# Kernel tuning notes

Measured on AMD Instinct MI355X. Metric: run time of the kernel, lower is better.

The kernel has to match this reference:

```python
import jax, jax.numpy as jnp
import numpy as np

INPUT, LATENT, HIDDEN, LAYERS = 64, 32, 128, 1
N, L = 256, 512


def setup_inputs() -> dict:
    key = jax.random.key(0)
    ks = jax.random.split(key, 12)
    s = 0.02
    inp = {
        "X": jax.random.normal(ks[0], (N, L, INPUT), jnp.float32),
        "eps_z": jax.random.normal(ks[1], (L, LAYERS, N, LATENT), jnp.float32),
        "eps_x": jax.random.normal(ks[2], (L, LAYERS, N, INPUT), jnp.float32),
        # qzcx: NormalModel(input+hidden -> latent): Linear to (mean, raw_std)
        "Wq": s * jax.random.normal(ks[3], (INPUT + HIDDEN, 2 * LATENT), jnp.float32),
        "bq": jnp.zeros((2 * LATENT,), jnp.float32),
        # pxcz: NormalModel(latent+hidden -> input)
        "Wp": s * jax.random.normal(ks[4], (LATENT + HIDDEN, 2 * INPUT), jnp.float32),
        "bp": jnp.zeros((2 * INPUT,), jnp.float32),
        # GRUCell(input+latent -> hidden), gates ordered (r, z, n) as in torch
        "W_ih": s * jax.random.normal(ks[5], (INPUT + LATENT, 3 * HIDDEN), jnp.float32),
        "W_hh": s * jax.random.normal(ks[6], (HIDDEN, 3 * HIDDEN), jnp.float32),
        "b_ih": jnp.zeros((3 * HIDDEN,), jnp.float32),
        "b_hh": jnp.zeros((3 * HIDDEN,), jnp.float32),
    }
    return inp


def _normal(x, W, b):
    # Linear head producing (mean, std) with softplus-positive std
    out = x @ W + b
    mean, raw = jnp.split(out, 2, axis=-1)
    return mean, jax.nn.softplus(raw)


def _gru(xcat, h, W_ih, W_hh, b_ih, b_hh):
    gi = xcat @ W_ih + b_ih
    gh = h @ W_hh + b_hh
    gi_r, gi_z, gi_n = jnp.split(gi, 3, axis=-1)
    gh_r, gh_z, gh_n = jnp.split(gh, 3, axis=-1)
    r = jax.nn.sigmoid(gi_r + gh_r)
    z = jax.nn.sigmoid(gi_z + gh_z)
    n = jnp.tanh(gi_n + r * gh_n)
    return (1.0 - z) * n + z * h


def reference(X, eps_z, eps_x, Wq, bq, Wp, bp, W_ih, W_hh, b_ih, b_hh):
    # X: [N, L, input] (batch_first). Recurrence over L via lax.scan.
    Xt = jnp.transpose(X, (1, 0, 2))  # [L, N, input]

    def cell(x, h, ez, ex):
        # one VRNNCell step (eval path); x:[N,In], h:[N,H]
        inf_mean, inf_std = _normal(jnp.concatenate([x, h], -1), Wq, bq)
        z_gen = inf_mean + inf_std * ez  # rsample
        x_mean, x_std = _normal(jnp.concatenate([z_gen, h], -1), Wp, bp)
        x_gen = x_mean + x_std * ex  # rsample
        return _gru(jnp.concatenate([x_gen, z_gen], -1), h, W_ih, W_hh, b_ih, b_hh)

    cell_layers = jax.vmap(cell, in_axes=(None, 0, 0, 0))  # over layer dim

    def step(hs, inputs):
        x, ez, ex = inputs
        new_hs = cell_layers(x, hs, ez, ex)  # [LAYERS, N, H]
        return new_hs, new_hs[-1]

    h0 = jnp.zeros((LAYERS, X.shape[0], HIDDEN), X.dtype)
    hs_final, outs = jax.lax.scan(step, h0, (Xt, eps_z, eps_x))
    output = jnp.transpose(outs, (1, 0, 2))  # [N, L, H] (batch_first)
    return output, hs_final
```

## Files before the change

kernel.cpp:

```cpp
#include <hip/hip_runtime.h>

namespace {

constexpr int NROWS = 256, LSTEPS = 512, IN = 64, LAT = 32, HID = 128;

typedef _Float16 h2 __attribute__((ext_vector_type(2)));
typedef _Float16 h8 __attribute__((ext_vector_type(8)));

__device__ __forceinline__ float fast_sigmoid(float x) {
    return __fdividef(1.f, 1.f + __expf(-x));
}
__device__ __forceinline__ float fast_softplus(float x) {
    return fmaxf(x, 0.f) + log1pf(__expf(-fabsf(x)));
}
__device__ __forceinline__ float fast_tanh(float x) {
    float e = __expf(-2.f * fabsf(x));
    float t = __fdividef(1.f - e, 1.f + e);
    return copysignf(t, x);
}

__device__ __forceinline__ float dot2f(h2 w, h2 a, float c) {
#if __has_builtin(__builtin_amdgcn_fdot2)
    return __builtin_amdgcn_fdot2(w, a, c, false);
#else
    return fmaf((float)w[0], (float)a[0], fmaf((float)w[1], (float)a[1], c));
#endif
}

__device__ __forceinline__ h2 packw(float a, float b) {
    h2 r; r[0] = (_Float16)a; r[1] = (_Float16)b; return r;
}

template<int BASE, int NPAIR>
__device__ __forceinline__ float dotp2(const _Float16* act, const h2 (&w)[120], float init) {
    float a0 = init, a1 = 0.f, a2 = 0.f, a3 = 0.f;
#pragma unroll
    for (int i = 0; i < NPAIR / 4; ++i) {
        h8 b = *(const h8*)(act + 8 * i);
        a0 = dot2f(w[BASE + 4 * i + 0], __builtin_shufflevector(b, b, 0, 1), a0);
        a1 = dot2f(w[BASE + 4 * i + 1], __builtin_shufflevector(b, b, 2, 3), a1);
        a2 = dot2f(w[BASE + 4 * i + 2], __builtin_shufflevector(b, b, 4, 5), a2);
        a3 = dot2f(w[BASE + 4 * i + 3], __builtin_shufflevector(b, b, 6, 7), a3);
    }
    return (a0 + a1) + (a2 + a3);
}

}

__global__ __launch_bounds__(512)
__attribute__((amdgpu_waves_per_eu(2, 2)))
void vrnn_kernel(
    const float* __restrict__ X, const float* __restrict__ EZ, const float* __restrict__ EX,
    const float* __restrict__ Wq, const float* __restrict__ bq,
    const float* __restrict__ Wp, const float* __restrict__ bp,
    const float* __restrict__ Wih, const float* __restrict__ Whh,
    const float* __restrict__ bih, const float* __restrict__ bhh,
    float* __restrict__ out)
{
    __shared__ alignas(16) _Float16 XH[192];
    __shared__ alignas(16) _Float16 ZH[32];
    __shared__ alignas(16) _Float16 XZ[64];
    __shared__ alignas(16) float gh_part[384][4];
    __shared__ alignas(16) float gi_part[384][8];

    const int t = threadIdx.x;
    const int n = blockIdx.x;

    h2 wpk[120];

    const int y = t - 256;

    int mg[3], kqg[3];
    int mx[3], kqx[3];
    int mz[3], khz[3];
#pragma unroll
    for (int i = 0; i < 3; ++i) {
        int s = (t < 256) ? (3 * t + i) : (768 + 3 * y + i);
        mg[i] = s >> 2; kqg[i] = s & 3;
        mx[i] = s >> 2; kqx[i] = s & 3;
        if (t >= 256) { int sz = 3 * y + i; mz[i] = sz >> 1; khz[i] = sz & 1; }
        else { mz[i] = 0; khz[i] = 0; }
    }

    if (t < 256) {
        const int j = t >> 2, sub = t & 3;
        const int o = (sub < 2) ? j : j + 64;
        const int kh = sub & 1;
#pragma unroll
        for (int p = 0; p < 32; ++p) { int k = 32 + 64 * kh + 2 * p;
            wpk[p] = packw(Wp[k * 128 + o], Wp[(k + 1) * 128 + o]); }
#pragma unroll
        for (int p = 0; p < 8; ++p) { int k = 16 * kh + 2 * p;
            wpk[32 + p] = packw(Wp[k * 128 + o], Wp[(k + 1) * 128 + o]); }
#pragma unroll
        for (int i = 0; i < 3; ++i)
#pragma unroll
            for (int p = 0; p < 16; ++p) { int k = 32 * kqg[i] + 2 * p;
                wpk[40 + 16 * i + p] = packw(Whh[k * 384 + mg[i]], Whh[(k + 1) * 384 + mg[i]]); }
#pragma unroll
        for (int i = 0; i < 3; ++i)
#pragma unroll
            for (int p = 0; p < 8; ++p) { int k = 16 * kqx[i] + 2 * p;
                wpk[88 + 8 * i + p] = packw(Wih[k * 384 + mx[i]], Wih[(k + 1) * 384 + mx[i]]); }
    } else {
        const int j = y >> 3, sub = y & 7;
        const int o = (sub < 4) ? j : j + 32;
        const int k0 = (sub & 3) * 48;
#pragma unroll
        for (int p = 0; p < 24; ++p) { int k = k0 + 2 * p;
            wpk[p] = packw(Wq[k * 64 + o], Wq[(k + 1) * 64 + o]); }
#pragma unroll
        for (int i = 0; i < 3; ++i)
#pragma unroll
            for (int p = 0; p < 16; ++p) { int k = 32 * kqg[i] + 2 * p;
                wpk[24 + 16 * i + p] = packw(Whh[k * 384 + mg[i]], Whh[(k + 1) * 384 + mg[i]]); }
#pragma unroll
        for (int i = 0; i < 3; ++i)
#pragma unroll
            for (int p = 0; p < 8; ++p) { int k = 64 + 16 * khz[i] + 2 * p;
                wpk[72 + 8 * i + p] = packw(Wih[k * 384 + mz[i]], Wih[(k + 1) * 384 + mz[i]]); }
#pragma unroll
        for (int i = 0; i < 3; ++i)
#pragma unroll
            for (int p = 0; p < 8; ++p) { int k = 16 * kqx[i] + 2 * p;
                wpk[96 + 8 * i + p] = packw(Wih[k * 384 + mx[i]], Wih[(k + 1) * 384 + mx[i]]); }
    }

    float bqm = 0.f, bqr = 0.f, bpm = 0.f, bpr = 0.f;
    float bir = 0.f, biz = 0.f, bin_ = 0.f, bhr = 0.f, bhz = 0.f, bhn = 0.f;
    if (t >= 256 && (y & 7) == 0) { bqm = bq[y >> 3]; bqr = bq[(y >> 3) + 32]; }
    if (t < 256 && (t & 3) == 0)  { bpm = bp[t >> 2]; bpr = bp[(t >> 2) + 64]; }
    if (t < 128) { bir = bih[t]; biz = bih[128 + t]; bin_ = bih[256 + t];
                   bhr = bhh[t]; bhz = bhh[128 + t]; bhn = bhh[256 + t]; }

    const float* Xrow = X + n * (LSTEPS * IN);
    float* orow = out + n * (LSTEPS * HID);
    float hreg = 0.f;
    if (t < 128) XH[64 + t] = (_Float16)0.f;
    if (t < 64)  XH[t] = (_Float16)Xrow[t];

    float ez_nxt = 0.f, ex_nxt = 0.f, xn_nxt = 0.f;
    if (t >= 256 && (y & 7) == 0) ez_nxt = EZ[n * LAT + (y >> 3)];
    if (t < 256 && (t & 3) == 0)  ex_nxt = EX[n * IN + (t >> 2)];
    __syncthreads();

    float ph = 0.f;

    for (int l = 0; l < LSTEPS; ++l) {
        const float ez_cur = ez_nxt, ex_cur = ex_nxt;
        if (l + 1 < LSTEPS) {
            if (t >= 256 && (y & 7) == 0) ez_nxt = EZ[(l + 1) * (NROWS * LAT) + n * LAT + (y >> 3)];
            if (t < 256 && (t & 3) == 0)  ex_nxt = EX[(l + 1) * (NROWS * IN) + n * IN + (t >> 2)];
            if (t < 64) xn_nxt = Xrow[(l + 1) * IN + t];
        }

        if (t < 256) {
            const int kh = t & 1;
            ph = dotp2<0, 32>(XH + 64 + 64 * kh, wpk, 0.f);
            float g0 = dotp2<40, 16>(XH + 64 + 32 * kqg[0], wpk, 0.f);
            float g1 = dotp2<56, 16>(XH + 64 + 32 * kqg[1], wpk, 0.f);
            float g2 = dotp2<72, 16>(XH + 64 + 32 * kqg[2], wpk, 0.f);
            gh_part[mg[0]][kqg[0]] = g0;
            gh_part[mg[1]][kqg[1]] = g1;
            gh_part[mg[2]][kqg[2]] = g2;
        } else {
            const int sub = y & 7, k0 = (sub & 3) * 48;
            float q = dotp2<0, 24>(XH + k0, wpk, 0.f);
            float g0 = dotp2<24, 16>(XH + 64 + 32 * kqg[0], wpk, 0.f);
            float g1 = dotp2<40, 16>(XH + 64 + 32 * kqg[1], wpk, 0.f);
            float g2 = dotp2<56, 16>(XH + 64 + 32 * kqg[2], wpk, 0.f);
            gh_part[mg[0]][kqg[0]] = g0;
            gh_part[mg[1]][kqg[1]] = g1;
            gh_part[mg[2]][kqg[2]] = g2;
            q += __shfl_xor(q, 1);
            q += __shfl_xor(q, 2);
            float other = __shfl_xor(q, 4);
            if (sub == 0) {
                float z = (q + bqm) + fast_softplus(other + bqr) * ez_cur;
                ZH[y >> 3] = (_Float16)z;
            }
        }
        __syncthreads();

        if (t < 256) {
            const int kh = t & 1, sub = t & 3;
            float tot = dotp2<32, 8>(ZH + 16 * kh, wpk, ph);
            tot += __shfl_xor(tot, 1);
            float other = __shfl_xor(tot, 2);
            if (sub == 0) {
                float xg = (tot + bpm) + fast_softplus(other + bpr) * ex_cur;
                XZ[t >> 2] = (_Float16)xg;
            }
        } else {
            gi_part[mz[0]][khz[0]] = dotp2<72, 8>(ZH + 16 * khz[0], wpk, 0.f);
            gi_part[mz[1]][khz[1]] = dotp2<80, 8>(ZH + 16 * khz[1], wpk, 0.f);
            gi_part[mz[2]][khz[2]] = dotp2<88, 8>(ZH + 16 * khz[2], wpk, 0.f);
        }
        __syncthreads();

        if (t < 256) {
            gi_part[mx[0]][2 + kqx[0]] = dotp2<88, 8>(XZ + 16 * kqx[0], wpk, 0.f);
            gi_part[mx[1]][2 + kqx[1]] = dotp2<96, 8>(XZ + 16 * kqx[1], wpk, 0.f);
            gi_part[mx[2]][2 + kqx[2]] = dotp2<104, 8>(XZ + 16 * kqx[2], wpk, 0.f);
            if (t < 64 && l + 1 < LSTEPS) XH[t] = (_Float16)xn_nxt;
        } else {
            gi_part[mx[0]][2 + kqx[0]] = dotp2<96, 8>(XZ + 16 * kqx[0], wpk, 0.f);
            gi_part[mx[1]][2 + kqx[1]] = dotp2<104, 8>(XZ + 16 * kqx[1], wpk, 0.f);
            gi_part[mx[2]][2 + kqx[2]] = dotp2<112, 8>(XZ + 16 * kqx[2], wpk, 0.f);
        }
        __syncthreads();

        if (t < 128) {
            float4 a; float2 b2;
            a = *(const float4*)&gi_part[t][0];        b2 = *(const float2*)&gi_part[t][4];
            float gir = (a.x + a.y) + (a.z + a.w) + (b2.x + b2.y) + bir;
            a = *(const float4*)&gi_part[128 + t][0];  b2 = *(const float2*)&gi_part[128 + t][4];
            float giz = (a.x + a.y) + (a.z + a.w) + (b2.x + b2.y) + biz;
            a = *(const float4*)&gi_part[256 + t][0];  b2 = *(const float2*)&gi_part[256 + t][4];
            float gin = (a.x + a.y) + (a.z + a.w) + (b2.x + b2.y) + bin_;
            a = *(const float4*)&gh_part[t][0];
            float ghr = (a.x + a.y) + (a.z + a.w) + bhr;
            a = *(const float4*)&gh_part[128 + t][0];
            float ghz = (a.x + a.y) + (a.z + a.w) + bhz;
            a = *(const float4*)&gh_part[256 + t][0];
            float ghn = (a.x + a.y) + (a.z + a.w) + bhn;
            float r  = fast_sigmoid(gir + ghr);
            float zg = fast_sigmoid(giz + ghz);
            float nn = fast_tanh(fmaf(r, ghn, gin));
            float hnew = fmaf(zg, hreg - nn, nn);
            hreg = hnew;
            XH[64 + t] = (_Float16)hnew;
            orow[l * HID + t] = hnew;
        }
        __syncthreads();
    }

    if (t < 128) out[NROWS * LSTEPS * HID + n * HID + t] = hreg;
}

extern "C" void kernel_launch(void* const* d_in, const int* in_sizes, int n_in,
                              void* d_out, int out_size, void* d_ws, size_t ws_size,
                              hipStream_t stream) {
    const float* X   = (const float*)d_in[0];
    const float* EZ  = (const float*)d_in[1];
    const float* EX  = (const float*)d_in[2];
    const float* Wq  = (const float*)d_in[3];
    const float* bq  = (const float*)d_in[4];
    const float* Wp  = (const float*)d_in[5];
    const float* bp  = (const float*)d_in[6];
    const float* Wih = (const float*)d_in[7];
    const float* Whh = (const float*)d_in[8];
    const float* bih = (const float*)d_in[9];
    const float* bhh = (const float*)d_in[10];
    float* out = (float*)d_out;

    vrnn_kernel<<<dim3(NROWS), dim3(512), 0, stream>>>(
        X, EZ, EX, Wq, bq, Wp, bp, Wih, Whh, bih, bhh, out);
}
```

Measured before the change: 1.023 ms.

## Double threads per block and halve per-thread register weights, rebalancing GRU work

Launches 1024 threads per batch row instead of 512 and cuts each thread's register-resident weight slice from 120 to 60 packed half2 values. Work is split across more lanes with deeper shuffle reductions. Part of the W_hh gate work moves from the first phase into the second phase to balance load. Softplus now uses __logf instead of log1pf. This shortens the per-thread dot products on the serial recurrence path. In exchange it adds more partial sums to reduce and may raise synchronisation cost across 16 waves.

```diff
diff --git a/kernel.cpp b/kernel.cpp
--- a/kernel.cpp
+++ b/kernel.cpp
@@ -11,14 +11,12 @@
     return __fdividef(1.f, 1.f + __expf(-x));
 }
 __device__ __forceinline__ float fast_softplus(float x) {
-    return fmaxf(x, 0.f) + log1pf(__expf(-fabsf(x)));
+    return fmaxf(x, 0.f) + __logf(1.f + __expf(-fabsf(x)));
 }
 __device__ __forceinline__ float fast_tanh(float x) {
     float e = __expf(-2.f * fabsf(x));
-    float t = __fdividef(1.f - e, 1.f + e);
-    return copysignf(t, x);
-}
-
+    return copysignf(__fdividef(1.f - e, 1.f + e), x);
+}
 __device__ __forceinline__ float dot2f(h2 w, h2 a, float c) {
 #if __has_builtin(__builtin_amdgcn_fdot2)
     return __builtin_amdgcn_fdot2(w, a, c, false);
@@ -26,13 +24,12 @@
     return fmaf((float)w[0], (float)a[0], fmaf((float)w[1], (float)a[1], c));
 #endif
 }
-
 __device__ __forceinline__ h2 packw(float a, float b) {
     h2 r; r[0] = (_Float16)a; r[1] = (_Float16)b; return r;
 }
 
 template<int BASE, int NPAIR>
-__device__ __forceinline__ float dotp2(const _Float16* act, const h2 (&w)[120], float init) {
+__device__ __forceinline__ float dotp2(const _Float16* act, const h2 (&w)[60], float init) {
     float a0 = init, a1 = 0.f, a2 = 0.f, a3 = 0.f;
 #pragma unroll
     for (int i = 0; i < NPAIR / 4; ++i) {
@@ -47,9 +44,7 @@
 
 }
 
-__global__ __launch_bounds__(512)
-__attribute__((amdgpu_waves_per_eu(2, 2)))
-void vrnn_kernel(
+__global__ __launch_bounds__(1024) void vrnn_kernel(
     const float* __restrict__ X, const float* __restrict__ EZ, const float* __restrict__ EX,
     const float* __restrict__ Wq, const float* __restrict__ bq,
     const float* __restrict__ Wp, const float* __restrict__ bp,
@@ -60,76 +55,75 @@
     __shared__ alignas(16) _Float16 XH[192];
     __shared__ alignas(16) _Float16 ZH[32];
     __shared__ alignas(16) _Float16 XZ[64];
-    __shared__ alignas(16) float gh_part[384][4];
-    __shared__ alignas(16) float gi_part[384][8];
+    __shared__ alignas(16) float gi_part[384][12];
+    __shared__ alignas(16) float gh_part[384][12];
 
     const int t = threadIdx.x;
     const int n = blockIdx.x;
-
-    h2 wpk[120];
-
-    const int y = t - 256;
-
-    int mg[3], kqg[3];
-    int mx[3], kqx[3];
-    int mz[3], khz[3];
+    const int y = t - 512;
+
+    h2 wpk[60];
+
+    int mh[3], k8h[3];
 #pragma unroll
     for (int i = 0; i < 3; ++i) {
-        int s = (t < 256) ? (3 * t + i) : (768 + 3 * y + i);
-        mg[i] = s >> 2; kqg[i] = s & 3;
-        mx[i] = s >> 2; kqx[i] = s & 3;
-        if (t >= 256) { int sz = 3 * y + i; mz[i] = sz >> 1; khz[i] = sz & 1; }
-        else { mz[i] = 0; khz[i] = 0; }
-    }
-
-    if (t < 256) {
-        const int j = t >> 2, sub = t & 3;
-        const int o = (sub < 2) ? j : j + 64;
-        const int kh = sub & 1;
-#pragma unroll
-        for (int p = 0; p < 32; ++p) { int k = 32 + 64 * kh + 2 * p;
+        int s = (t < 512) ? (3 * t + i) : (1536 + 3 * y + i);
+        mh[i] = s >> 3; k8h[i] = s & 7;
+    }
+    int mxA = 0, kxA = 0, mxB = 0, kxB = 0;
+    if (t < 512) { mxA = t >> 2; kxA = t & 3; int s = 1024 + t; mxB = s >> 2; kxB = s & 3; }
+    else         { int s = 512 + y; mxA = s >> 2; kxA = s & 3; }
+    int mzA = 0, kzA = 0, mzB = 0, kzB = 0;
+    if (t >= 512) { mzA = y >> 1; kzA = y & 1; int s = 512 + y; mzB = s >> 1; kzB = s & 1; }
+
+    if (t < 512) {
+        const int j = t >> 3, mr = (t >> 2) & 1, kq = t & 3;
+        const int o = j + mr * 64;
+#pragma unroll
+        for (int p = 0; p < 16; ++p) { int k = 32 + kq * 32 + 2 * p;
             wpk[p] = packw(Wp[k * 128 + o], Wp[(k + 1) * 128 + o]); }
 #pragma unroll
-        for (int p = 0; p < 8; ++p) { int k = 16 * kh + 2 * p;
-            wpk[32 + p] = packw(Wp[k * 128 + o], Wp[(k + 1) * 128 + o]); }
+        for (int p = 0; p < 4; ++p) { int k = kq * 8 + 2 * p;
+            wpk[16 + p] = packw(Wp[k * 128 + o], Wp[(k + 1) * 128 + o]); }
 #pragma unroll
         for (int i = 0; i < 3; ++i)
 #pragma unroll
-            for (int p = 0; p < 16; ++p) { int k = 32 * kqg[i] + 2 * p;
-                wpk[40 + 16 * i + p] = packw(Whh[k * 384 + mg[i]], Whh[(k + 1) * 384 + mg[i]]); }
+            for (int p = 0; p < 8; ++p) { int k = 16 * k8h[i] + 2 * p;
+                wpk[20 + 8 * i + p] = packw(Whh[k * 384 + mh[i]], Whh[(k + 1) * 384 + mh[i]]); }
+#pragma unroll
+        for (int p = 0; p < 8; ++p) { int k = 16 * kxA + 2 * p;
+            wpk[44 + p] = packw(Wih[k * 384 + mxA], Wih[(k + 1) * 384 + mxA]); }
+#pragma unroll
+        for (int p = 0; p < 8; ++p) { int k = 16 * kxB + 2 * p;
+            wpk[52 + p] = packw(Wih[k * 384 + mxB], Wih[(k + 1) * 384 + mxB]); }
+    } else {
+        const int j = y >> 4, mr = (y >> 3) & 1, k3 = y & 7;
+        const int o = j + mr * 32;
+#pragma unroll
+        for (int p = 0; p < 12; ++p) { int k = 24 * k3 + 2 * p;
+            wpk[p] = packw(Wq[k * 64 + o], Wq[(k + 1) * 64 + o]); }
 #pragma unroll
         for (int i = 0; i < 3; ++i)
 #pragma unroll
-            for (int p = 0; p < 8; ++p) { int k = 16 * kqx[i] + 2 * p;
-                wpk[88 + 8 * i + p] = packw(Wih[k * 384 + mx[i]], Wih[(k + 1) * 384 + mx[i]]); }
-    } else {
-        const int j = y >> 3, sub = y & 7;
-        const int o = (sub < 4) ? j : j + 32;
-        const int k0 = (sub & 3) * 48;
-#pragma unroll
-        for (int p = 0; p < 24; ++p) { int k = k0 + 2 * p;
-            wpk[p] = packw(Wq[k * 64 + o], Wq[(k + 1) * 64 + o]); }
-#pragma unroll
-        for (int i = 0; i < 3; ++i)
-#pragma unroll
-            for (int p = 0; p < 16; ++p) { int k = 32 * kqg[i] + 2 * p;
-                wpk[24 + 16 * i + p] = packw(Whh[k * 384 + mg[i]], Whh[(k + 1) * 384 + mg[i]]); }
-#pragma unroll
-        for (int i = 0; i < 3; ++i)
-#pragma unroll
-            for (int p = 0; p < 8; ++p) { int k = 64 + 16 * khz[i] + 2 * p;
-                wpk[72 + 8 * i + p] = packw(Wih[k * 384 + mz[i]], Wih[(k + 1) * 384 + mz[i]]); }
-#pragma unroll
-        for (int i = 0; i < 3; ++i)
-#pragma unroll
-            for (int p = 0; p < 8; ++p) { int k = 16 * kqx[i] + 2 * p;
-                wpk[96 + 8 * i + p] = packw(Wih[k * 384 + mx[i]], Wih[(k + 1) * 384 + mx[i]]); }
+            for (int p = 0; p < 8; ++p) { int k = 16 * k8h[i] + 2 * p;
+                wpk[12 + 8 * i + p] = packw(Whh[k * 384 + mh[i]], Whh[(k + 1) * 384 + mh[i]]); }
+#pragma unroll
+        for (int p = 0; p < 8; ++p) { int k = 64 + 16 * kzA + 2 * p;
+            wpk[36 + p] = packw(Wih[k * 384 + mzA], Wih[(k + 1) * 384 + mzA]); }
+        if (y < 256) {
+#pragma unroll
+            for (int p = 0; p < 8; ++p) { int k = 64 + 16 * kzB + 2 * p;
+                wpk[44 + p] = packw(Wih[k * 384 + mzB], Wih[(k + 1) * 384 + mzB]); }
+        }
+#pragma unroll
+        for (int p = 0; p < 8; ++p) { int k = 16 * kxA + 2 * p;
+            wpk[52 + p] = packw(Wih[k * 384 + mxA], Wih[(k + 1) * 384 + mxA]); }
     }
 
     float bqm = 0.f, bqr = 0.f, bpm = 0.f, bpr = 0.f;
     float bir = 0.f, biz = 0.f, bin_ = 0.f, bhr = 0.f, bhz = 0.f, bhn = 0.f;
-    if (t >= 256 && (y & 7) == 0) { bqm = bq[y >> 3]; bqr = bq[(y >> 3) + 32]; }
-    if (t < 256 && (t & 3) == 0)  { bpm = bp[t >> 2]; bpr = bp[(t >> 2) + 64]; }
+    if (t >= 512 && (y & 15) == 0) { bqm = bq[y >> 4]; bqr = bq[(y >> 4) + 32]; }
+    if (t < 512 && (t & 7) == 0)   { bpm = bp[t >> 3]; bpr = bp[(t >> 3) + 64]; }
     if (t < 128) { bir = bih[t]; biz = bih[128 + t]; bin_ = bih[256 + t];
                    bhr = bhh[t]; bhz = bhh[128 + t]; bhn = bhh[256 + t]; }
 
@@ -140,8 +134,8 @@
     if (t < 64)  XH[t] = (_Float16)Xrow[t];
 
     float ez_nxt = 0.f, ex_nxt = 0.f, xn_nxt = 0.f;
-    if (t >= 256 && (y & 7) == 0) ez_nxt = EZ[n * LAT + (y >> 3)];
-    if (t < 256 && (t & 3) == 0)  ex_nxt = EX[n * IN + (t >> 2)];
+    if (t >= 512 && (y & 15) == 0) ez_nxt = EZ[n * LAT + (y >> 4)];
+    if (t < 512 && (t & 7) == 0)   ex_nxt = EX[n * IN + (t >> 3)];
     __syncthreads();
 
     float ph = 0.f;
@@ -149,64 +143,69 @@
     for (int l = 0; l < LSTEPS; ++l) {
         const float ez_cur = ez_nxt, ex_cur = ex_nxt;
         if (l + 1 < LSTEPS) {
-            if (t >= 256 && (y & 7) == 0) ez_nxt = EZ[(l + 1) * (NROWS * LAT) + n * LAT + (y >> 3)];
-            if (t < 256 && (t & 3) == 0)  ex_nxt = EX[(l + 1) * (NROWS * IN) + n * IN + (t >> 2)];
+            if (t >= 512 && (y & 15) == 0) ez_nxt = EZ[(l + 1) * (NROWS * LAT) + n * LAT + (y >> 4)];
+            if (t < 512 && (t & 7) == 0)   ex_nxt = EX[(l + 1) * (NROWS * IN) + n * IN + (t >> 3)];
             if (t < 64) xn_nxt = Xrow[(l + 1) * IN + t];
         }
 
-        if (t < 256) {
-            const int kh = t & 1;
-            ph = dotp2<0, 32>(XH + 64 + 64 * kh, wpk, 0.f);
-            float g0 = dotp2<40, 16>(XH + 64 + 32 * kqg[0], wpk, 0.f);
-            float g1 = dotp2<56, 16>(XH + 64 + 32 * kqg[1], wpk, 0.f);
-            float g2 = dotp2<72, 16>(XH + 64 + 32 * kqg[2], wpk, 0.f);
-            gh_part[mg[0]][kqg[0]] = g0;
-            gh_part[mg[1]][kqg[1]] = g1;
-            gh_part[mg[2]][kqg[2]] = g2;
+        if (t < 512) {
+            const int kq = t & 3;
+            ph = dotp2<0, 16>(XH + 64 + 32 * kq, wpk, 0.f);
+            float g0 = dotp2<20, 8>(XH + 64 + 16 * k8h[0], wpk, 0.f);
+            float g1 = dotp2<28, 8>(XH + 64 + 16 * k8h[1], wpk, 0.f);
+            gh_part[mh[0]][k8h[0]] = g0;
+            gh_part[mh[1]][k8h[1]] = g1;
         } else {
-            const int sub = y & 7, k0 = (sub & 3) * 48;
-            float q = dotp2<0, 24>(XH + k0, wpk, 0.f);
-            float g0 = dotp2<24, 16>(XH + 64 + 32 * kqg[0], wpk, 0.f);
-            float g1 = dotp2<40, 16>(XH + 64 + 32 * kqg[1], wpk, 0.f);
-            float g2 = dotp2<56, 16>(XH + 64 + 32 * kqg[2], wpk, 0.f);
-            gh_part[mg[0]][kqg[0]] = g0;
-            gh_part[mg[1]][kqg[1]] = g1;
-            gh_part[mg[2]][kqg[2]] = g2;
+            const int k3 = y & 7;
+            float q = dotp2<0, 12>(XH + 24 * k3, wpk, 0.f);
             q += __shfl_xor(q, 1);
             q += __shfl_xor(q, 2);
-            float other = __shfl_xor(q, 4);
-            if (sub == 0) {
+            q += __shfl_xor(q, 4);
+            float other = __shfl_xor(q, 8);
+            float g0 = dotp2<12, 8>(XH + 64 + 16 * k8h[0], wpk, 0.f);
+            float g1 = dotp2<20, 8>(XH + 64 + 16 * k8h[1], wpk, 0.f);
+            gh_part[mh[0]][k8h[0]] = g0;
+            gh_part[mh[1]][k8h[1]] = g1;
+            if ((y & 15) == 0) {
                 float z = (q + bqm) + fast_softplus(other + bqr) * ez_cur;
-                ZH[y >> 3] = (_Float16)z;
+                ZH[y >> 4] = (_Float16)z;
             }
         }
         __syncthreads();
 
-        if (t < 256) {
-            const int kh = t & 1, sub = t & 3;
-            float tot = dotp2<32, 8>(ZH + 16 * kh, wpk, ph);
+        if (t < 512) {
+            const int kq = t & 3;
+            float tot = dotp2<16, 4>(ZH + 8 * kq, wpk, ph);
             tot += __shfl_xor(tot, 1);
-            float other = __shfl_xor(tot, 2);
-            if (sub == 0) {
+            tot += __shfl_xor(tot, 2);
+            float other = __shfl_xor(tot, 4);
+            float g2 = dotp2<36, 8>(XH + 64 + 16 * k8h[2], wpk, 0.f);
+            gh_part[mh[2]][k8h[2]] = g2;
+            if ((t & 7) == 0) {
                 float xg = (tot + bpm) + fast_softplus(other + bpr) * ex_cur;
-                XZ[t >> 2] = (_Float16)xg;
+                XZ[t >> 3] = (_Float16)xg;
             }
         } else {
-            gi_part[mz[0]][khz[0]] = dotp2<72, 8>(ZH + 16 * khz[0], wpk, 0.f);
-            gi_part[mz[1]][khz[1]] = dotp2<80, 8>(ZH + 16 * khz[1], wpk, 0.f);
-            gi_part[mz[2]][khz[2]] = dotp2<88, 8>(ZH + 16 * khz[2], wpk, 0.f);
-        }
-        __syncthreads();
-
-        if (t < 256) {
-            gi_part[mx[0]][2 + kqx[0]] = dotp2<88, 8>(XZ + 16 * kqx[0], wpk, 0.f);
-            gi_part[mx[1]][2 + kqx[1]] = dotp2<96, 8>(XZ + 16 * kqx[1], wpk, 0.f);
-            gi_part[mx[2]][2 + kqx[2]] = dotp2<104, 8>(XZ + 16 * kqx[2], wpk, 0.f);
+            float z0 = dotp2<36, 8>(ZH + 16 * kzA, wpk, 0.f);
+            gi_part[mzA][4 + kzA] = z0;
+            if (y < 256) {
+                float z1 = dotp2<44, 8>(ZH + 16 * kzB, wpk, 0.f);
+                gi_part[mzB][4 + kzB] = z1;
+            }
+            float g2 = dotp2<28, 8>(XH + 64 + 16 * k8h[2], wpk, 0.f);
+            gh_part[mh[2]][k8h[2]] = g2;
+        }
+        __syncthreads();
+
+        if (t < 512) {
+            float x0 = dotp2<44, 8>(XZ + 16 * kxA, wpk, 0.f);
+            float x1 = dotp2<52, 8>(XZ + 16 * kxB, wpk, 0.f);
+            gi_part[mxA][kxA] = x0;
+            gi_part[mxB][kxB] = x1;
             if (t < 64 && l + 1 < LSTEPS) XH[t] = (_Float16)xn_nxt;
         } else {
-            gi_part[mx[0]][2 + kqx[0]] = dotp2<96, 8>(XZ + 16 * kqx[0], wpk, 0.f);
-            gi_part[mx[1]][2 + kqx[1]] = dotp2<104, 8>(XZ + 16 * kqx[1], wpk, 0.f);
-            gi_part[mx[2]][2 + kqx[2]] = dotp2<112, 8>(XZ + 16 * kqx[2], wpk, 0.f);
+            float x2 = dotp2<52, 8>(XZ + 16 * kxA, wpk, 0.f);
+            gi_part[mxA][kxA] = x2;
         }
         __syncthreads();
 
@@ -218,12 +217,13 @@
             float giz = (a.x + a.y) + (a.z + a.w) + (b2.x + b2.y) + biz;
             a = *(const float4*)&gi_part[256 + t][0];  b2 = *(const float2*)&gi_part[256 + t][4];
             float gin = (a.x + a.y) + (a.z + a.w) + (b2.x + b2.y) + bin_;
-            a = *(const float4*)&gh_part[t][0];
-            float ghr = (a.x + a.y) + (a.z + a.w) + bhr;
-            a = *(const float4*)&gh_part[128 + t][0];
-            float ghz = (a.x + a.y) + (a.z + a.w) + bhz;
-            a = *(const float4*)&gh_part[256 + t][0];
-            float ghn = (a.x + a.y) + (a.z + a.w) + bhn;
+            float4 c4, d4;
+            c4 = *(const float4*)&gh_part[t][0];       d4 = *(const float4*)&gh_part[t][4];
+            float ghr = ((c4.x + c4.y) + (c4.z + c4.w)) + ((d4.x + d4.y) + (d4.z + d4.w)) + bhr;
+            c4 = *(const float4*)&gh_part[128 + t][0]; d4 = *(const float4*)&gh_part[128 + t][4];
+            float ghz = ((c4.x + c4.y) + (c4.z + c4.w)) + ((d4.x + d4.y) + (d4.z + d4.w)) + bhz;
+            c4 = *(const float4*)&gh_part[256 + t][0]; d4 = *(const float4*)&gh_part[256 + t][4];
+            float ghn = ((c4.x + c4.y) + (c4.z + c4.w)) + ((d4.x + d4.y) + (d4.z + d4.w)) + bhn;
             float r  = fast_sigmoid(gir + ghr);
             float zg = fast_sigmoid(giz + ghz);
             float nn = fast_tanh(fmaf(r, ghn, gin));
@@ -254,6 +254,6 @@
     const float* bhh = (const float*)d_in[10];
     float* out = (float*)d_out;
 
-    vrnn_kernel<<<dim3(NROWS), dim3(512), 0, stream>>>(
+    vrnn_kernel<<<dim3(NROWS), dim3(1024), 0, stream>>>(
         X, EZ, EX, Wq, bq, Wp, bp, Wih, Whh, bih, bhh, out);
 }
```

After: 1.013 ms. About the same (-0.9%).
